# Optimization experiments

Measured on AMD Instinct MI355X. Metric: run time of the kernel, lower is better.

Reference implementation:

```python
import jax, jax.numpy as jnp
import numpy as np
import math

NUM_HEADS = 16


def build_hier_idx(seq_len):
    """Vectorized port of build_hierarchical_index_lookup_table.
    Returns [seq_len, log2(seq_len)] int32 neighbor indices into the
    concatenated [leaves | internal nodes] array of length 2*seq_len-1.
    For power-of-two seq_len every entry is valid (no -1s)."""
    assert seq_len & (seq_len - 1) == 0
    level_num = int(math.log2(seq_len))
    cur = np.arange(seq_len, dtype=np.int64)
    cols = []
    for lvl in range(level_num):
        if lvl == 0:
            nxt = cur ^ 1
        else:
            nxt = (cur // 2 + seq_len) ^ 1  # python precedence: (cur//2 + seq_len) ^ 1
        cols.append(nxt)
        cur = nxt
    return np.stack(cols, axis=1)  # [seq_len, level_num]


def setup_inputs() -> dict:
    key = jax.random.key(0)
    ks = jax.random.split(key, 9)
    B, N, D = 2, 2048, 1024
    s = 1.0 / math.sqrt(D)
    return {
        "query": jax.random.normal(ks[0], (B, N, D), jnp.float32),
        "key": jax.random.normal(ks[1], (B, N, D), jnp.float32),
        "value": jax.random.normal(ks[2], (B, N, D), jnp.float32),
        "y": jax.random.normal(ks[3], (B, N - 1, D), jnp.float32),
        "Wq": jax.random.normal(ks[4], (D, D), jnp.float32) * s,
        "Wk": jax.random.normal(ks[5], (D, D), jnp.float32) * s,
        "Wv": jax.random.normal(ks[6], (D, D), jnp.float32) * s,
        "Wo": jax.random.normal(ks[7], (D, D), jnp.float32) * s,
        "bo": jax.random.normal(ks[8], (D,), jnp.float32) * 0.01,
    }


def reference(query, key, value, y, Wq, Wk, Wv, Wo, bo):
    # Sparse path: L_Q == L_K == L_V and y is not None -> update_X_from_Y + out_proj_x.
    # key/value are unused in this branch (only their lengths are checked).
    B, N, D = query.shape
    H = NUM_HEADS
    Dh = D // H
    scale = 1.0 / math.sqrt(Dh)

    idx = jnp.asarray(build_hier_idx(N))          # [N, Lv], Lv = log2(N)

    xy = jnp.concatenate([query, y], axis=1)      # [B, 2N-1, D]
    Q = (query @ Wq.T).reshape(B, N, H, Dh).transpose(0, 2, 1, 3)   # [B,H,N,Dh]
    Kf = (xy @ Wk.T).reshape(B, -1, H, Dh).transpose(0, 2, 1, 3)    # [B,H,2N-1,Dh]
    Vf = (xy @ Wv.T).reshape(B, -1, H, Dh).transpose(0, 2, 1, 3)

    K_self = Kf[:, :, :N, :]                      # [B,H,N,Dh]
    V_self = Vf[:, :, :N, :]
    Kn = Kf[:, :, idx, :]                         # [B,H,N,Lv,Dh] gather over tree levels
    Vn = Vf[:, :, idx, :]

    self_logits = jnp.einsum('bhnd,bhnd->bhn', Q, K_self) * scale          # [B,H,N]
    nbr_logits = jnp.einsum('bhnd,bhnld->bhnl', Q, Kn) * scale             # [B,H,N,Lv]

    all_logits = jnp.concatenate([self_logits[..., None], nbr_logits], axis=-1)  # [B,H,N,1+Lv]
    all_v = jnp.concatenate([V_self[:, :, :, None, :], Vn], axis=3)              # [B,H,N,1+Lv,Dh]

    w = jax.nn.softmax(all_logits, axis=-1)
    out = jnp.einsum('bhnl,bhnld->bhnd', w, all_v)                               # [B,H,N,Dh]
    out = out.transpose(0, 2, 1, 3).reshape(B, N, D)
    return out @ Wo.T + bo
```

## Files before the change

kernel.cpp:

```cpp
#include <hip/hip_runtime.h>
#include <hip/hip_bf16.h>
#include <cstdint>
#include <cstddef>

#define B_ 2
#define N_ 2048
#define D_ 1024
#define H_ 16
#define DH_ 64
#define XYROWS 4095
#define NL 12
#define QKVN 3072

typedef __attribute__((ext_vector_type(8))) short bf16x8;
typedef __attribute__((ext_vector_type(4))) float f32x4;

__device__ __forceinline__ float asf(unsigned int u) {
    union { unsigned int i; float f; } v; v.i = u; return v.f;
}
__device__ __forceinline__ unsigned short f2bf(float f) {
    union { float f; unsigned int i; } v; v.f = f;
    unsigned int u = v.i;
    unsigned int r = u + 0x7FFFu + ((u >> 16) & 1u);
    return (unsigned short)(r >> 16);
}

__device__ __forceinline__ void ld8(const unsigned short* p, float* o) {
    uint4 u = *(const uint4*)p;
    o[0] = asf(u.x << 16); o[1] = asf(u.x & 0xffff0000u);
    o[2] = asf(u.y << 16); o[3] = asf(u.y & 0xffff0000u);
    o[4] = asf(u.z << 16); o[5] = asf(u.z & 0xffff0000u);
    o[6] = asf(u.w << 16); o[7] = asf(u.w & 0xffff0000u);
}

__device__ __forceinline__ void gload_lds16(const unsigned short* g, unsigned short* l) {
    __builtin_amdgcn_global_load_lds(
        (const __attribute__((address_space(1))) unsigned int*)g,
        (__attribute__((address_space(3))) unsigned int*)l,
        16, 0, 0);
}

__global__ void prep_kernel(const float* __restrict__ q, const float* __restrict__ y,
                            const float* __restrict__ Wq, const float* __restrict__ Wk,
                            const float* __restrict__ Wv, const float* __restrict__ Wo,
                            unsigned short* __restrict__ xy,
                            unsigned short* __restrict__ wqkv, unsigned short* __restrict__ wob) {
    int c = blockIdx.x * blockDim.x + threadIdx.x;
    constexpr int TOTAL_XY = B_ * XYROWS * (D_ / 8);
    constexpr int TOTAL_W  = 4 * 131072;
    if (c >= TOTAL_XY + TOTAL_W) return;
    const float* src;
    unsigned short* dst;
    if (c < TOTAL_XY) {
        int col8 = (c & (D_ / 8 - 1)) * 8;
        int rg = c >> 7;
        int b = (rg >= XYROWS) ? 1 : 0;
        int r = rg - b * XYROWS;
        if (r < N_) src = q + ((size_t)b * N_ + r) * D_ + col8;
        else        src = y + ((size_t)b * (N_ - 1) + (r - N_)) * D_ + col8;
        dst = xy + (size_t)rg * D_ + col8;
    } else {
        int idx = c - TOTAL_XY;
        int which = idx >> 17;
        int sub = idx & 131071;
        const float* w = (which == 0) ? Wq : (which == 1) ? Wk : (which == 2) ? Wv : Wo;
        src = w + (size_t)sub * 8;
        dst = ((which < 3) ? (wqkv + (size_t)which * D_ * D_) : wob) + (size_t)sub * 8;
    }
    float4 a = *(const float4*)(src);
    float4 bb = *(const float4*)(src + 4);
    union { unsigned short us[8]; uint4 u4; } o;
    o.us[0] = f2bf(a.x);  o.us[1] = f2bf(a.y);  o.us[2] = f2bf(a.z);  o.us[3] = f2bf(a.w);
    o.us[4] = f2bf(bb.x); o.us[5] = f2bf(bb.y); o.us[6] = f2bf(bb.z); o.us[7] = f2bf(bb.w);
    *(uint4*)(dst) = o.u4;
}

template<int BM, bool OUTF32, bool BIAS, bool QSKIP>
__global__ __launch_bounds__(256, 2)
void gemm_bt(const unsigned short* __restrict__ A, const unsigned short* __restrict__ W,
             void* __restrict__ Cv, const float* __restrict__ bias, int M, int Nn) {
    constexpr int K = 1024, BK = 64;
    constexpr int IM = BM / 32;
    __shared__ __align__(16) unsigned short la[BM * 64];
    __shared__ __align__(16) unsigned short lb[128 * 64];

    int row0 = blockIdx.x * BM;
    if (row0 >= M) return;
    int col0 = blockIdx.y * 128;
    if (QSKIP && col0 < 1024) {
        int t = blockIdx.x;
        if ((t >= 16 && t <= 30) || t >= 48) return;
    }
    int tid = threadIdx.x;
    int wave = tid >> 6, lane = tid & 63;
    int wm = wave >> 1, wn = wave & 1;
    int q4 = lane >> 4, r = lane & 15;

    int rsub = lane >> 3;
    int csw = ((lane & 7) ^ rsub) * 8;

    f32x4 acc[IM][4];
    f32x4 zero = {0.f, 0.f, 0.f, 0.f};
#pragma unroll
    for (int i = 0; i < IM; i++)
#pragma unroll
        for (int j = 0; j < 4; j++) acc[i][j] = zero;

    for (int k0 = 0; k0 < K; k0 += BK) {
#pragma unroll
        for (int p = 0; p < IM; p++) {
            int seg = wave * IM + p;
            int ar = row0 + seg * 8 + rsub; if (ar >= M) ar = M - 1;
            gload_lds16(A + (size_t)ar * K + k0 + csw, &la[seg * 512]);
        }
#pragma unroll
        for (int p = 0; p < 4; p++) {
            int seg = wave * 4 + p;
            gload_lds16(W + (size_t)(col0 + seg * 8 + rsub) * K + k0 + csw, &lb[seg * 512]);
        }
        __syncthreads();
#pragma unroll
        for (int ks = 0; ks < 2; ks++) {
            int cidx = ks * 4 + q4;
            bf16x8 af[IM], bfv[4];
#pragma unroll
            for (int j = 0; j < 4; j++) {
                int rb = wn * 64 + j * 16 + r;
                bfv[j] = *(const bf16x8*)(&lb[rb * 64 + ((cidx ^ (rb & 7)) << 3)]);
            }
#pragma unroll
            for (int i = 0; i < IM; i++) {
                int rr = wm * (BM / 2) + i * 16 + r;
                af[i] = *(const bf16x8*)(&la[rr * 64 + ((cidx ^ (rr & 7)) << 3)]);
            }
#pragma unroll
            for (int i = 0; i < IM; i++)
#pragma unroll
                for (int j = 0; j < 4; j++)
                    acc[i][j] = __builtin_amdgcn_mfma_f32_16x16x32_bf16(af[i], bfv[j], acc[i][j], 0, 0, 0);
        }
        __syncthreads();
    }

    float bv[4];
    if (BIAS) {
#pragma unroll
        for (int j = 0; j < 4; j++) bv[j] = bias[col0 + wn * 64 + j * 16 + r];
    }
#pragma unroll
    for (int i = 0; i < IM; i++) {
#pragma unroll
        for (int j = 0; j < 4; j++) {
            int col = col0 + wn * 64 + j * 16 + r;
#pragma unroll
            for (int reg = 0; reg < 4; reg++) {
                int row = row0 + wm * (BM / 2) + i * 16 + q4 * 4 + reg;
                if (row < M) {
                    float v = acc[i][j][reg];
                    if (BIAS) v += bv[j];
                    if (OUTF32)
                        ((float*)Cv)[(size_t)row * Nn + col] = v;
                    else
                        ((unsigned short*)Cv)[(size_t)row * Nn + col] = f2bf(v);
                }
            }
        }
    }
}

__global__ __launch_bounds__(256)
void attn_kernel(const unsigned short* __restrict__ QKV, unsigned short* __restrict__ O) {
    int t = threadIdx.x;
    int pi = (blockIdx.x << 1) | (t >> 7);
    int c = t & 127;
    int b = blockIdx.y;
    int n0 = pi * 2;

    int rows[NL];
    rows[0] = n0;
    rows[1] = n0 + 1;
    int cur = n0 + 1;
#pragma unroll
    for (int l = 1; l < 11; l++) {
        cur = ((cur >> 1) + N_) ^ 1;
        rows[l + 1] = cur;
    }

    const unsigned short* base = QKV + (size_t)b * XYROWS * QKVN;
    size_t c8 = (size_t)c * 8;

    float q0[8], q1[8];
    ld8(base + (size_t)n0 * QKVN + c8, q0);
    ld8(base + ((size_t)n0 + 1) * QKVN + c8, q1);

    float l0[NL], l1[NL];
#pragma unroll
    for (int j = 0; j < NL; j++) {
        float kv[8];
        ld8(base + (size_t)rows[j] * QKVN + D_ + c8, kv);
        float p0 = 0.f, p1 = 0.f;
#pragma unroll
        for (int e = 0; e < 8; e++) { p0 = fmaf(q0[e], kv[e], p0); p1 = fmaf(q1[e], kv[e], p1); }
        p0 += __shfl_xor(p0, 1); p1 += __shfl_xor(p1, 1);
        p0 += __shfl_xor(p0, 2); p1 += __shfl_xor(p1, 2);
        p0 += __shfl_xor(p0, 4); p1 += __shfl_xor(p1, 4);
        l0[j] = p0 * 0.125f;
        l1[j] = p1 * 0.125f;
    }

    float mx0 = l0[0], mx1 = l1[0];
#pragma unroll
    for (int j = 1; j < NL; j++) { mx0 = fmaxf(mx0, l0[j]); mx1 = fmaxf(mx1, l1[j]); }
    float s0 = 0.f, s1 = 0.f;
#pragma unroll
    for (int j = 0; j < NL; j++) {
        l0[j] = __expf(l0[j] - mx0); s0 += l0[j];
        l1[j] = __expf(l1[j] - mx1); s1 += l1[j];
    }
    float i0 = 1.f / s0, i1 = 1.f / s1;

    float a0[8] = {0,0,0,0,0,0,0,0}, a1[8] = {0,0,0,0,0,0,0,0};
#pragma unroll
    for (int j = 0; j < NL; j++) {
        float vv[8];
        ld8(base + (size_t)rows[j] * QKVN + 2 * D_ + c8, vv);
        float w0 = l0[j] * i0, w1 = l1[j] * i1;
#pragma unroll
        for (int e = 0; e < 8; e++) { a0[e] = fmaf(w0, vv[e], a0[e]); a1[e] = fmaf(w1, vv[e], a1[e]); }
    }

    union { unsigned short us[8]; uint4 u4; } o0, o1;
#pragma unroll
    for (int e = 0; e < 8; e++) { o0.us[e] = f2bf(a0[e]); o1.us[e] = f2bf(a1[e]); }
    size_t obase = ((size_t)b * N_ + n0) * D_ + c8;
    *(uint4*)(O + obase) = o0.u4;
    *(uint4*)(O + obase + D_) = o1.u4;
}

extern "C" void kernel_launch(void* const* d_in, const int* in_sizes, int n_in,
                              void* d_out, int out_size, void* d_ws, size_t ws_size,
                              hipStream_t stream) {
    const float* query = (const float*)d_in[0];
    const float* y  = (const float*)d_in[3];
    const float* Wq = (const float*)d_in[4];
    const float* Wk = (const float*)d_in[5];
    const float* Wv = (const float*)d_in[6];
    const float* Wo = (const float*)d_in[7];
    const float* bo = (const float*)d_in[8];
    float* out = (float*)d_out;

    char* ws = (char*)d_ws;
    size_t off = 0;
    auto alloc = [&](size_t bytes) {
        void* p = ws + off; off += (bytes + 255) & ~(size_t)255; return p;
    };
    unsigned short* xy   = (unsigned short*)alloc((size_t)B_ * XYROWS * D_ * 2 + 8192);
    unsigned short* wqkv = (unsigned short*)alloc((size_t)QKVN * D_ * 2);
    unsigned short* wob  = (unsigned short*)alloc((size_t)D_ * D_ * 2);
    unsigned short* QKV  = (unsigned short*)alloc((size_t)B_ * XYROWS * QKVN * 2 + 16384);
    unsigned short* At   = (unsigned short*)alloc((size_t)B_ * N_ * D_ * 2);

    prep_kernel<<<6144, 256, 0, stream>>>(query, y, Wq, Wk, Wv, Wo, xy, wqkv, wob);

    {
        dim3 g(64, QKVN / 128);
        gemm_bt<128, false, false, true><<<g, 256, 0, stream>>>(
            xy, wqkv, QKV, nullptr, B_ * XYROWS, QKVN);
    }
    {
        dim3 g(N_ / 4, B_);
        attn_kernel<<<g, 256, 0, stream>>>(QKV, At);
    }
    {
        dim3 g((B_ * N_) / 64, D_ / 128);
        gemm_bt<64, true, true, false><<<g, 256, 0, stream>>>(At, wob, out, bo, B_ * N_, D_);
    }
}
```

Measured before the change: 201.6 us.

## Double-buffer GEMM A tile, load B to registers, share tree K/V across four queries

```diff
diff --git a/kernel.cpp b/kernel.cpp
--- a/kernel.cpp
+++ b/kernel.cpp
@@ -79,10 +79,9 @@
 __global__ __launch_bounds__(256, 2)
 void gemm_bt(const unsigned short* __restrict__ A, const unsigned short* __restrict__ W,
              void* __restrict__ Cv, const float* __restrict__ bias, int M, int Nn) {
-    constexpr int K = 1024, BK = 64;
+    constexpr int K = 1024, BK = 64, NIT = K / BK;
     constexpr int IM = BM / 32;
-    __shared__ __align__(16) unsigned short la[BM * 64];
-    __shared__ __align__(16) unsigned short lb[128 * 64];
+    __shared__ __align__(16) unsigned short la[2][BM * 64];
 
     int row0 = blockIdx.x * BM;
     if (row0 >= M) return;
@@ -99,6 +98,8 @@
     int rsub = lane >> 3;
     int csw = ((lane & 7) ^ rsub) * 8;
 
+    const unsigned short* wp = W + (size_t)(col0 + wn * 64 + r) * K + q4 * 8;
+
     f32x4 acc[IM][4];
     f32x4 zero = {0.f, 0.f, 0.f, 0.f};
 #pragma unroll
@@ -106,40 +107,49 @@
 #pragma unroll
         for (int j = 0; j < 4; j++) acc[i][j] = zero;
 
-    for (int k0 = 0; k0 < K; k0 += BK) {
+    bf16x8 bfv[2][2][4];
+
+    auto stageA = [&](int k0, int buf) {
 #pragma unroll
         for (int p = 0; p < IM; p++) {
             int seg = wave * IM + p;
             int ar = row0 + seg * 8 + rsub; if (ar >= M) ar = M - 1;
-            gload_lds16(A + (size_t)ar * K + k0 + csw, &la[seg * 512]);
-        }
-#pragma unroll
-        for (int p = 0; p < 4; p++) {
-            int seg = wave * 4 + p;
-            gload_lds16(W + (size_t)(col0 + seg * 8 + rsub) * K + k0 + csw, &lb[seg * 512]);
-        }
+            gload_lds16(A + (size_t)ar * K + k0 + csw, &la[buf][seg * 512]);
+        }
+    };
+    auto loadB = [&](int k0, int buf) {
+#pragma unroll
+        for (int ks = 0; ks < 2; ks++)
+#pragma unroll
+            for (int j = 0; j < 4; j++)
+                bfv[buf][ks][j] = *(const bf16x8*)(wp + (size_t)(j * 16) * K + k0 + ks * 32);
+    };
+
+    stageA(0, 0);
+    loadB(0, 0);
+#pragma unroll
+    for (int it = 0; it < NIT; it++) {
+        int cur = it & 1;
         __syncthreads();
+        if (it + 1 < NIT) {
+            stageA((it + 1) * BK, cur ^ 1);
+            loadB((it + 1) * BK, cur ^ 1);
+        }
 #pragma unroll
         for (int ks = 0; ks < 2; ks++) {
             int cidx = ks * 4 + q4;
-            bf16x8 af[IM], bfv[4];
-#pragma unroll
-            for (int j = 0; j < 4; j++) {
-                int rb = wn * 64 + j * 16 + r;
-                bfv[j] = *(const bf16x8*)(&lb[rb * 64 + ((cidx ^ (rb & 7)) << 3)]);
-            }
+            bf16x8 af[IM];
 #pragma unroll
             for (int i = 0; i < IM; i++) {
                 int rr = wm * (BM / 2) + i * 16 + r;
-                af[i] = *(const bf16x8*)(&la[rr * 64 + ((cidx ^ (rr & 7)) << 3)]);
+                af[i] = *(const bf16x8*)(&la[cur][rr * 64 + ((cidx ^ (rr & 7)) << 3)]);
             }
 #pragma unroll
             for (int i = 0; i < IM; i++)
 #pragma unroll
                 for (int j = 0; j < 4; j++)
-                    acc[i][j] = __builtin_amdgcn_mfma_f32_16x16x32_bf16(af[i], bfv[j], acc[i][j], 0, 0, 0);
-        }
-        __syncthreads();
+                    acc[i][j] = __builtin_amdgcn_mfma_f32_16x16x32_bf16(af[i], bfv[cur][ks][j], acc[i][j], 0, 0, 0);
+        }
     }
 
     float bv[4];
@@ -171,70 +181,130 @@
 __global__ __launch_bounds__(256)
 void attn_kernel(const unsigned short* __restrict__ QKV, unsigned short* __restrict__ O) {
     int t = threadIdx.x;
-    int pi = (blockIdx.x << 1) | (t >> 7);
+    int b = blockIdx.y;
+    int u = (blockIdx.x << 1) | (t >> 7);
     int c = t & 127;
-    int b = blockIdx.y;
-    int n0 = pi * 2;
-
-    int rows[NL];
-    rows[0] = n0;
-    rows[1] = n0 + 1;
-    int cur = n0 + 1;
-#pragma unroll
-    for (int l = 1; l < 11; l++) {
-        cur = ((cur >> 1) + N_) ^ 1;
-        rows[l + 1] = cur;
-    }
+    int n0 = u << 2;
+
+    int rows[15];
+    rows[0] = n0; rows[1] = n0 + 1; rows[2] = n0 + 2; rows[3] = n0 + 3;
+    rows[4] = 2048 + 2 * u + 1;
+    rows[5] = 2048 + 2 * u;
+    int cur = (3072 + u) ^ 1;
+    rows[6] = cur;
+#pragma unroll
+    for (int l = 7; l < 15; l++) { cur = ((cur >> 1) + N_) ^ 1; rows[l] = cur; }
 
     const unsigned short* base = QKV + (size_t)b * XYROWS * QKVN;
     size_t c8 = (size_t)c * 8;
 
-    float q0[8], q1[8];
-    ld8(base + (size_t)n0 * QKVN + c8, q0);
-    ld8(base + ((size_t)n0 + 1) * QKVN + c8, q1);
-
-    float l0[NL], l1[NL];
-#pragma unroll
-    for (int j = 0; j < NL; j++) {
-        float kv[8];
-        ld8(base + (size_t)rows[j] * QKVN + D_ + c8, kv);
-        float p0 = 0.f, p1 = 0.f;
-#pragma unroll
-        for (int e = 0; e < 8; e++) { p0 = fmaf(q0[e], kv[e], p0); p1 = fmaf(q1[e], kv[e], p1); }
-        p0 += __shfl_xor(p0, 1); p1 += __shfl_xor(p1, 1);
-        p0 += __shfl_xor(p0, 2); p1 += __shfl_xor(p1, 2);
-        p0 += __shfl_xor(p0, 4); p1 += __shfl_xor(p1, 4);
-        l0[j] = p0 * 0.125f;
-        l1[j] = p1 * 0.125f;
-    }
-
-    float mx0 = l0[0], mx1 = l1[0];
-#pragma unroll
-    for (int j = 1; j < NL; j++) { mx0 = fmaxf(mx0, l0[j]); mx1 = fmaxf(mx1, l1[j]); }
-    float s0 = 0.f, s1 = 0.f;
-#pragma unroll
-    for (int j = 0; j < NL; j++) {
-        l0[j] = __expf(l0[j] - mx0); s0 += l0[j];
-        l1[j] = __expf(l1[j] - mx1); s1 += l1[j];
-    }
-    float i0 = 1.f / s0, i1 = 1.f / s1;
-
-    float a0[8] = {0,0,0,0,0,0,0,0}, a1[8] = {0,0,0,0,0,0,0,0};
-#pragma unroll
-    for (int j = 0; j < NL; j++) {
-        float vv[8];
-        ld8(base + (size_t)rows[j] * QKVN + 2 * D_ + c8, vv);
-        float w0 = l0[j] * i0, w1 = l1[j] * i1;
-#pragma unroll
-        for (int e = 0; e < 8; e++) { a0[e] = fmaf(w0, vv[e], a0[e]); a1[e] = fmaf(w1, vv[e], a1[e]); }
-    }
-
-    union { unsigned short us[8]; uint4 u4; } o0, o1;
-#pragma unroll
-    for (int e = 0; e < 8; e++) { o0.us[e] = f2bf(a0[e]); o1.us[e] = f2bf(a1[e]); }
-    size_t obase = ((size_t)b * N_ + n0) * D_ + c8;
-    *(uint4*)(O + obase) = o0.u4;
-    *(uint4*)(O + obase + D_) = o1.u4;
+    float q[4][8];
+#pragma unroll
+    for (int i = 0; i < 4; i++) ld8(base + (size_t)(n0 + i) * QKVN + c8, q[i]);
+
+    float lg[4][NL];
+    float kv[8];
+
+#pragma unroll
+    for (int i = 0; i < 4; i++) {
+        ld8(base + (size_t)rows[i] * QKVN + D_ + c8, kv);
+        int pa = i & 2, io = i & 1;
+        float s0 = 0.f, s1 = 0.f;
+#pragma unroll
+        for (int e = 0; e < 8; e++) { s0 = fmaf(q[pa][e], kv[e], s0); s1 = fmaf(q[pa + 1][e], kv[e], s1); }
+        s0 += __shfl_xor(s0, 1); s1 += __shfl_xor(s1, 1);
+        s0 += __shfl_xor(s0, 2); s1 += __shfl_xor(s1, 2);
+        s0 += __shfl_xor(s0, 4); s1 += __shfl_xor(s1, 4);
+        lg[pa][io] = s0 * 0.125f;
+        lg[pa + 1][io ^ 1] = s1 * 0.125f;
+    }
+#pragma unroll
+    for (int i = 4; i < 6; i++) {
+        ld8(base + (size_t)rows[i] * QKVN + D_ + c8, kv);
+        int pa = (i == 4) ? 0 : 2;
+        float s0 = 0.f, s1 = 0.f;
+#pragma unroll
+        for (int e = 0; e < 8; e++) { s0 = fmaf(q[pa][e], kv[e], s0); s1 = fmaf(q[pa + 1][e], kv[e], s1); }
+        s0 += __shfl_xor(s0, 1); s1 += __shfl_xor(s1, 1);
+        s0 += __shfl_xor(s0, 2); s1 += __shfl_xor(s1, 2);
+        s0 += __shfl_xor(s0, 4); s1 += __shfl_xor(s1, 4);
+        lg[pa][2] = s0 * 0.125f;
+        lg[pa + 1][2] = s1 * 0.125f;
+    }
+#pragma unroll
+    for (int i = 6; i < 15; i++) {
+        ld8(base + (size_t)rows[i] * QKVN + D_ + c8, kv);
+        float s0 = 0.f, s1 = 0.f, s2 = 0.f, s3 = 0.f;
+#pragma unroll
+        for (int e = 0; e < 8; e++) {
+            s0 = fmaf(q[0][e], kv[e], s0); s1 = fmaf(q[1][e], kv[e], s1);
+            s2 = fmaf(q[2][e], kv[e], s2); s3 = fmaf(q[3][e], kv[e], s3);
+        }
+        s0 += __shfl_xor(s0, 1); s1 += __shfl_xor(s1, 1); s2 += __shfl_xor(s2, 1); s3 += __shfl_xor(s3, 1);
+        s0 += __shfl_xor(s0, 2); s1 += __shfl_xor(s1, 2); s2 += __shfl_xor(s2, 2); s3 += __shfl_xor(s3, 2);
+        s0 += __shfl_xor(s0, 4); s1 += __shfl_xor(s1, 4); s2 += __shfl_xor(s2, 4); s3 += __shfl_xor(s3, 4);
+        lg[0][i - 3] = s0 * 0.125f; lg[1][i - 3] = s1 * 0.125f;
+        lg[2][i - 3] = s2 * 0.125f; lg[3][i - 3] = s3 * 0.125f;
+    }
+
+    float inv[4];
+#pragma unroll
+    for (int qi = 0; qi < 4; qi++) {
+        float mx = lg[qi][0];
+#pragma unroll
+        for (int j = 1; j < NL; j++) mx = fmaxf(mx, lg[qi][j]);
+        float s = 0.f;
+#pragma unroll
+        for (int j = 0; j < NL; j++) { lg[qi][j] = __expf(lg[qi][j] - mx); s += lg[qi][j]; }
+        inv[qi] = 1.f / s;
+    }
+
+    float acc[4][8];
+#pragma unroll
+    for (int qi = 0; qi < 4; qi++)
+#pragma unroll
+        for (int e = 0; e < 8; e++) acc[qi][e] = 0.f;
+
+#pragma unroll
+    for (int i = 0; i < 4; i++) {
+        ld8(base + (size_t)rows[i] * QKVN + 2 * D_ + c8, kv);
+        int pa = i & 2, io = i & 1;
+        float w0 = lg[pa][io], w1 = lg[pa + 1][io ^ 1];
+#pragma unroll
+        for (int e = 0; e < 8; e++) {
+            acc[pa][e] = fmaf(w0, kv[e], acc[pa][e]);
+            acc[pa + 1][e] = fmaf(w1, kv[e], acc[pa + 1][e]);
+        }
+    }
+#pragma unroll
+    for (int i = 4; i < 6; i++) {
+        ld8(base + (size_t)rows[i] * QKVN + 2 * D_ + c8, kv);
+        int pa = (i == 4) ? 0 : 2;
+        float w0 = lg[pa][2], w1 = lg[pa + 1][2];
+#pragma unroll
+        for (int e = 0; e < 8; e++) {
+            acc[pa][e] = fmaf(w0, kv[e], acc[pa][e]);
+            acc[pa + 1][e] = fmaf(w1, kv[e], acc[pa + 1][e]);
+        }
+    }
+#pragma unroll
+    for (int i = 6; i < 15; i++) {
+        ld8(base + (size_t)rows[i] * QKVN + 2 * D_ + c8, kv);
+#pragma unroll
+        for (int qi = 0; qi < 4; qi++) {
+            float w = lg[qi][i - 3];
+#pragma unroll
+            for (int e = 0; e < 8; e++) acc[qi][e] = fmaf(w, kv[e], acc[qi][e]);
+        }
+    }
+
+#pragma unroll
+    for (int qi = 0; qi < 4; qi++) {
+        union { unsigned short us[8]; uint4 u4; } o;
+#pragma unroll
+        for (int e = 0; e < 8; e++) o.us[e] = f2bf(acc[qi][e] * inv[qi]);
+        *(uint4*)(O + ((size_t)b * N_ + n0 + qi) * D_ + c8) = o.u4;
+    }
 }
 
 extern "C" void kernel_launch(void* const* d_in, const int* in_sizes, int n_in,
@@ -255,8 +325,8 @@
         void* p = ws + off; off += (bytes + 255) & ~(size_t)255; return p;
     };
     unsigned short* xy   = (unsigned short*)alloc((size_t)B_ * XYROWS * D_ * 2 + 8192);
-    unsigned short* wqkv = (unsigned short*)alloc((size_t)QKVN * D_ * 2);
-    unsigned short* wob  = (unsigned short*)alloc((size_t)D_ * D_ * 2);
+    unsigned short* wqkv = (unsigned short*)alloc((size_t)QKVN * D_ * 2 + 8192);
+    unsigned short* wob  = (unsigned short*)alloc((size_t)D_ * D_ * 2 + 8192);
     unsigned short* QKV  = (unsigned short*)alloc((size_t)B_ * XYROWS * QKVN * 2 + 16384);
     unsigned short* At   = (unsigned short*)alloc((size_t)B_ * N_ * D_ * 2);
 
@@ -268,7 +338,7 @@
             xy, wqkv, QKV, nullptr, B_ * XYROWS, QKVN);
     }
     {
-        dim3 g(N_ / 4, B_);
+        dim3 g(N_ / 8, B_);
         attn_kernel<<<g, 256, 0, stream>>>(QKV, At);
     }
     {
```

New measurement: 274.3 us. 1.36x slower.
